# Kernel optimization log

Measured on AMD Instinct MI355X. Metric: run time of the kernel, lower is better.

Reference implementation:

```python
import jax, jax.numpy as jnp
import numpy as np

HUGE = 1e9  # stand-in for ops.HUGE_INT


def setup_inputs() -> dict:
    key = jax.random.key(0)
    ks = jax.random.split(key, 8)
    B, Q, K = 8, 128, 256
    Dq = Dk = Dv = H = 512
    query = jax.random.normal(ks[0], (B, Q, Dq), dtype=jnp.float32)
    k_ = jax.random.normal(ks[1], (B, K, Dk), dtype=jnp.float32)
    value = jax.random.normal(ks[2], (B, K, Dv), dtype=jnp.float32)
    mask = jax.random.randint(ks[3], (B, K), 0, 2, dtype=jnp.int32)
    # FFN params: linear1 (Dq+Dk -> H, bias), linear2 (H -> 1, no bias)
    W1 = jax.random.normal(ks[4], (Dq + Dk, H), dtype=jnp.float32) * 0.05
    b1 = jax.random.normal(ks[5], (H,), dtype=jnp.float32) * 0.05
    w2 = jax.random.normal(ks[6], (H, 1), dtype=jnp.float32) * 0.05
    return {"query": query, "key": k_, "value": value, "mask": mask,
            "W1": W1, "b1": b1, "w2": w2}


def reference(query, key, value, mask, W1, b1, w2):
    # Additive (FFN) attention. Original tiles query/key into [B, Q*K, Dq+Dk]
    # and applies linear1; concat@W1 is separable, so we project q and k
    # separately and broadcast-add (same math, no tiled concat tensor).
    Dq = query.shape[-1]
    Wq, Wk = W1[:Dq], W1[Dq:]
    q_proj = jnp.einsum('bqd,dh->bqh', query, Wq)   # [B,Q,H]
    k_proj = jnp.einsum('bkd,dh->bkh', key, Wk)     # [B,K,H]
    hidden = jnp.tanh(q_proj[:, :, None, :] + k_proj[:, None, :, :] + b1)  # [B,Q,K,H]
    scores = jnp.einsum('bqkh,h->bqk', hidden, w2[:, 0])  # [B,Q,K]
    # padding mask fill BEFORE scaling, matching the original op order
    scores = jnp.where(mask[:, None, :] != 0, -HUGE, scores)
    scores = scores / jnp.sqrt(jnp.float32(key.shape[-1]))
    attn_weights = jax.nn.softmax(scores, axis=-1)
    attn_vec = jnp.einsum('bqk,bkv->bqv', attn_weights, value)  # dropout=0 at eval
    return attn_vec, attn_weights
```

## Files before the change

kernel.cpp:

```cpp
#include <hip/hip_runtime.h>
#include <hip/hip_bf16.h>

#define B_ 8
#define Q_ 128
#define K_ 256
#define D_ 512
#define TWOLOG2E 2.8853900817779268f
#define SCALE 0.044194173824159216f
#define L2E 1.4426950408889634f
#define MASKVAL (-44194173.824159216f)

typedef __attribute__((ext_vector_type(8))) short frag8;
typedef __attribute__((ext_vector_type(4))) float f32x4;

__device__ __forceinline__ float fexp2(float x) {
  float r;
  asm("v_exp_f32 %0, %1" : "=v"(r) : "v"(x));
  return r;
}
__device__ __forceinline__ float frcp(float x) {
  float r;
  asm("v_rcp_f32 %0, %1" : "=v"(r) : "v"(x));
  return r;
}
__device__ __forceinline__ unsigned f2bf_u(float x) {
  unsigned u = __float_as_uint(x);
  return (u + 0x7FFFu + ((u >> 16) & 1u)) >> 16;
}
__device__ __forceinline__ unsigned short f2bf(float x) {
  return (unsigned short)f2bf_u(x);
}
__device__ __forceinline__ unsigned packbf(float lo, float hi) {
  return f2bf_u(lo) | (f2bf_u(hi) << 16);
}

__global__ __launch_bounds__(256) void gemm_kernel(
    const float* __restrict__ query, const float* __restrict__ key,
    const float* __restrict__ W1, const float* __restrict__ b1,
    float* __restrict__ qp, float* __restrict__ kpbT) {
  __shared__ short As[32 * 64];
  __shared__ short Bs[64 * 72];
  const int t = threadIdx.x;
  const int m0 = blockIdx.y * 32;
  const int n0 = blockIdx.x * 64;
  const bool is_k = (m0 >= B_ * Q_);
  const float* X = is_k ? key : query;
  const int xrow0 = is_k ? (m0 - B_ * Q_) : m0;
  const float* Wb = W1 + (is_k ? (size_t)D_ * D_ : 0);

  const int am = t >> 3;
  const int ac = t & 7;
  const float* gA = X + (size_t)(xrow0 + am) * D_ + ac * 8;
  short* aw = As + am * 64 + ((ac ^ (am & 7)) * 8);

  const int prow = t >> 4;
  const int n4 = (t & 15) * 4;
  const float* gB = Wb + n0 + n4;

  const int l = t & 63;
  const int w = t >> 6;
  const int lr = l & 15;
  const int kg = l >> 4;
  const int key8 = lr & 7;
  int aoff[2][2], boff[2];
#pragma unroll
  for (int kk = 0; kk < 2; ++kk) {
    const int cposA = ((kg + kk * 4) ^ key8) * 8;
#pragma unroll
    for (int mt = 0; mt < 2; ++mt) aoff[mt][kk] = (mt * 16 + lr) * 64 + cposA;
    boff[kk] = (w * 16 + lr) * 72 + (kg + kk * 4) * 8;
  }

  f32x4 acc[2];
  acc[0] = (f32x4){0.f, 0.f, 0.f, 0.f};
  acc[1] = (f32x4){0.f, 0.f, 0.f, 0.f};

  for (int k0 = 0; k0 < D_; k0 += 64) {
    float4 a0 = *(const float4*)(gA + k0);
    float4 a1 = *(const float4*)(gA + k0 + 4);
    float4 w00 = *(const float4*)(gB + (size_t)(k0 + 2 * prow) * D_);
    float4 w01 = *(const float4*)(gB + (size_t)(k0 + 2 * prow + 1) * D_);
    float4 w10 = *(const float4*)(gB + (size_t)(k0 + 2 * prow + 32) * D_);
    float4 w11 = *(const float4*)(gB + (size_t)(k0 + 2 * prow + 33) * D_);
    __syncthreads();
    {
      union { frag8 f; unsigned short u[8]; } av;
      av.u[0] = f2bf(a0.x); av.u[1] = f2bf(a0.y); av.u[2] = f2bf(a0.z); av.u[3] = f2bf(a0.w);
      av.u[4] = f2bf(a1.x); av.u[5] = f2bf(a1.y); av.u[6] = f2bf(a1.z); av.u[7] = f2bf(a1.w);
      *(frag8*)aw = av.f;
    }
    {
      float lo0[4] = {w00.x, w00.y, w00.z, w00.w};
      float hi0[4] = {w01.x, w01.y, w01.z, w01.w};
      float lo1[4] = {w10.x, w10.y, w10.z, w10.w};
      float hi1[4] = {w11.x, w11.y, w11.z, w11.w};
#pragma unroll
      for (int j = 0; j < 4; ++j) {
        *(unsigned*)(Bs + (n4 + j) * 72 + 2 * prow) = packbf(lo0[j], hi0[j]);
        *(unsigned*)(Bs + (n4 + j) * 72 + 2 * (prow + 16)) = packbf(lo1[j], hi1[j]);
      }
    }
    __syncthreads();
#pragma unroll
    for (int kk = 0; kk < 2; ++kk) {
      frag8 bf = *(const frag8*)(Bs + boff[kk]);
#pragma unroll
      for (int mt = 0; mt < 2; ++mt) {
        frag8 af = *(const frag8*)(As + aoff[mt][kk]);
        acc[mt] = __builtin_amdgcn_mfma_f32_16x16x32_bf16(af, bf, acc[mt], 0, 0, 0);
      }
    }
  }

  const int col = n0 + w * 16 + lr;
  if (is_k) {
    const float bc = b1[col];
#pragma unroll
    for (int mt = 0; mt < 2; ++mt) {
      const int krow = m0 - B_ * Q_ + mt * 16 + kg * 4;
      const int bb = krow >> 8;
      const int kk0 = krow & 255;
      float4 v;
      v.x = fexp2((acc[mt][0] + bc) * TWOLOG2E);
      v.y = fexp2((acc[mt][1] + bc) * TWOLOG2E);
      v.z = fexp2((acc[mt][2] + bc) * TWOLOG2E);
      v.w = fexp2((acc[mt][3] + bc) * TWOLOG2E);
      *(float4*)&kpbT[((size_t)bb * D_ + col) * K_ + kk0] = v;
    }
  } else {
#pragma unroll
    for (int mt = 0; mt < 2; ++mt) {
#pragma unroll
      for (int i = 0; i < 4; ++i) {
        const int row = m0 + mt * 16 + kg * 4 + i;
        qp[(size_t)row * D_ + col] = fexp2(acc[mt][i] * TWOLOG2E);
      }
    }
  }
}

__global__ __launch_bounds__(1024) void attn_kernel(
    const float* __restrict__ qp, const float* __restrict__ kpbT,
    const float* __restrict__ value, const int* __restrict__ mask,
    const float* __restrict__ w2,
    float* __restrict__ out_vec, float* __restrict__ out_w) {
  __shared__ float smem_p[16 * 512];
  __shared__ float pw[4 * 256];
  const int bid = blockIdx.x;
  const int b = bid & 7;
  const int q0 = (bid >> 3) * 4;
  const int t = threadIdx.x;
  const int lane = t & 63;
  const int w = __builtin_amdgcn_readfirstlane(t >> 6);
  const int kc = w & 1;
  const int hq = w >> 1;
  const int h0 = hq * 64;

  {
    const float* pk = kpbT + ((size_t)b * D_ + h0) * K_ + kc * 128 + 2 * lane;
    const float* q_0 = qp + (size_t)(b * Q_ + q0 + 0) * D_ + h0;
    const float* q_1 = qp + (size_t)(b * Q_ + q0 + 1) * D_ + h0;
    const float* q_2 = qp + (size_t)(b * Q_ + q0 + 2) * D_ + h0;
    const float* q_3 = qp + (size_t)(b * Q_ + q0 + 3) * D_ + h0;
    const float* w2h = w2 + h0;

    float2 a0 = {0.f, 0.f}, a1 = {0.f, 0.f}, a2 = {0.f, 0.f}, a3 = {0.f, 0.f};
    for (int h = 0; h < 64; h += 8) {
      float2 kv[8];
#pragma unroll
      for (int j = 0; j < 8; ++j) kv[j] = *(const float2*)&pk[(size_t)(h + j) * K_];
      float4 e0a = *(const float4*)(q_0 + h), e0b = *(const float4*)(q_0 + h + 4);
      float4 e1a = *(const float4*)(q_1 + h), e1b = *(const float4*)(q_1 + h + 4);
      float4 e2a = *(const float4*)(q_2 + h), e2b = *(const float4*)(q_2 + h + 4);
      float4 e3a = *(const float4*)(q_3 + h), e3b = *(const float4*)(q_3 + h + 4);
      float4 wa = *(const float4*)(w2h + h), wb = *(const float4*)(w2h + h + 4);
      float E0[8] = {e0a.x, e0a.y, e0a.z, e0a.w, e0b.x, e0b.y, e0b.z, e0b.w};
      float E1[8] = {e1a.x, e1a.y, e1a.z, e1a.w, e1b.x, e1b.y, e1b.z, e1b.w};
      float E2[8] = {e2a.x, e2a.y, e2a.z, e2a.w, e2b.x, e2b.y, e2b.z, e2b.w};
      float E3[8] = {e3a.x, e3a.y, e3a.z, e3a.w, e3b.x, e3b.y, e3b.z, e3b.w};
      float WV[8] = {wa.x, wa.y, wa.z, wa.w, wb.x, wb.y, wb.z, wb.w};
#pragma unroll
      for (int p = 0; p < 4; ++p) {
        const int j0 = 2 * p, j1 = 2 * p + 1;
        const float w0 = WV[j0], w1 = WV[j1];
        {
          float d0x = fmaf(E0[j0], kv[j0].x, 1.f), d1x = fmaf(E0[j1], kv[j1].x, 1.f);
          float d0y = fmaf(E0[j0], kv[j0].y, 1.f), d1y = fmaf(E0[j1], kv[j1].y, 1.f);
          a0.x = fmaf(fmaf(w0, d1x, w1 * d0x), frcp(d0x * d1x), a0.x);
          a0.y = fmaf(fmaf(w0, d1y, w1 * d0y), frcp(d0y * d1y), a0.y);
        }
        {
          float d0x = fmaf(E1[j0], kv[j0].x, 1.f), d1x = fmaf(E1[j1], kv[j1].x, 1.f);
          float d0y = fmaf(E1[j0], kv[j0].y, 1.f), d1y = fmaf(E1[j1], kv[j1].y, 1.f);
          a1.x = fmaf(fmaf(w0, d1x, w1 * d0x), frcp(d0x * d1x), a1.x);
          a1.y = fmaf(fmaf(w0, d1y, w1 * d0y), frcp(d0y * d1y), a1.y);
        }
        {
          float d0x = fmaf(E2[j0], kv[j0].x, 1.f), d1x = fmaf(E2[j1], kv[j1].x, 1.f);
          float d0y = fmaf(E2[j0], kv[j0].y, 1.f), d1y = fmaf(E2[j1], kv[j1].y, 1.f);
          a2.x = fmaf(fmaf(w0, d1x, w1 * d0x), frcp(d0x * d1x), a2.x);
          a2.y = fmaf(fmaf(w0, d1y, w1 * d0y), frcp(d0y * d1y), a2.y);
        }
        {
          float d0x = fmaf(E3[j0], kv[j0].x, 1.f), d1x = fmaf(E3[j1], kv[j1].x, 1.f);
          float d0y = fmaf(E3[j0], kv[j0].y, 1.f), d1y = fmaf(E3[j1], kv[j1].y, 1.f);
          a3.x = fmaf(fmaf(w0, d1x, w1 * d0x), frcp(d0x * d1x), a3.x);
          a3.y = fmaf(fmaf(w0, d1y, w1 * d0y), frcp(d0y * d1y), a3.y);
        }
      }
    }
    *(float2*)&smem_p[w * 512 + 0 * 128 + 2 * lane] = a0;
    *(float2*)&smem_p[w * 512 + 1 * 128 + 2 * lane] = a1;
    *(float2*)&smem_p[w * 512 + 2 * 128 + 2 * lane] = a2;
    *(float2*)&smem_p[w * 512 + 3 * 128 + 2 * lane] = a3;
  }
  __syncthreads();

  if (w < 4) {
    const int q = w;
    float sw = 0.f;
#pragma unroll
    for (int m = 0; m < 8; ++m) sw += w2[lane + 64 * m];
#pragma unroll
    for (int off = 32; off; off >>= 1) sw += __shfl_xor(sw, off);

    float s[4];
#pragma unroll
    for (int r = 0; r < 4; ++r) {
      const int kcc = r >> 1;
      const int off = (r & 1) * 64 + lane;
      float p = 0.f;
#pragma unroll
      for (int hh = 0; hh < 8; ++hh)
        p += smem_p[(hh * 2 + kcc) * 512 + q * 128 + off];
      const int mk = mask[b * K_ + r * 64 + lane];
      s[r] = mk ? MASKVAL : fmaf(-2.f, p, sw) * SCALE;
    }
    float mx = fmaxf(fmaxf(s[0], s[1]), fmaxf(s[2], s[3]));
#pragma unroll
    for (int off = 32; off; off >>= 1) mx = fmaxf(mx, __shfl_xor(mx, off));
    float e[4], sum = 0.f;
#pragma unroll
    for (int r = 0; r < 4; ++r) {
      e[r] = fexp2((s[r] - mx) * L2E);
      sum += e[r];
    }
#pragma unroll
    for (int off = 32; off; off >>= 1) sum += __shfl_xor(sum, off);
    const float inv = frcp(sum);
    float* ow = out_w + (size_t)(b * Q_ + q0 + q) * K_;
#pragma unroll
    for (int r = 0; r < 4; ++r) {
      const float p = e[r] * inv;
      pw[q * 256 + r * 64 + lane] = p;
      ow[r * 64 + lane] = p;
    }
  }
  __syncthreads();

  {
    const int cp = t & 255;
    const int col = cp * 2;
    const int kq = t >> 8;
    const float* vb = value + (size_t)b * K_ * D_ + (size_t)(kq * 64) * D_ + col;
    const float* pwq = pw + kq * 64;

    float2 o0 = {0.f, 0.f}, o1 = {0.f, 0.f}, o2 = {0.f, 0.f}, o3 = {0.f, 0.f};
    for (int k0 = 0; k0 < 64; k0 += 4) {
      const float4 P0 = *(const float4*)&pwq[0 * 256 + k0];
      const float4 P1 = *(const float4*)&pwq[1 * 256 + k0];
      const float4 P2 = *(const float4*)&pwq[2 * 256 + k0];
      const float4 P3 = *(const float4*)&pwq[3 * 256 + k0];
      const float2 v0 = *(const float2*)&vb[(size_t)(k0 + 0) * D_];
      const float2 v1 = *(const float2*)&vb[(size_t)(k0 + 1) * D_];
      const float2 v2 = *(const float2*)&vb[(size_t)(k0 + 2) * D_];
      const float2 v3 = *(const float2*)&vb[(size_t)(k0 + 3) * D_];
      o0.x = fmaf(P0.x, v0.x, fmaf(P0.y, v1.x, fmaf(P0.z, v2.x, fmaf(P0.w, v3.x, o0.x))));
      o0.y = fmaf(P0.x, v0.y, fmaf(P0.y, v1.y, fmaf(P0.z, v2.y, fmaf(P0.w, v3.y, o0.y))));
      o1.x = fmaf(P1.x, v0.x, fmaf(P1.y, v1.x, fmaf(P1.z, v2.x, fmaf(P1.w, v3.x, o1.x))));
      o1.y = fmaf(P1.x, v0.y, fmaf(P1.y, v1.y, fmaf(P1.z, v2.y, fmaf(P1.w, v3.y, o1.y))));
      o2.x = fmaf(P2.x, v0.x, fmaf(P2.y, v1.x, fmaf(P2.z, v2.x, fmaf(P2.w, v3.x, o2.x))));
      o2.y = fmaf(P2.x, v0.y, fmaf(P2.y, v1.y, fmaf(P2.z, v2.y, fmaf(P2.w, v3.y, o2.y))));
      o3.x = fmaf(P3.x, v0.x, fmaf(P3.y, v1.x, fmaf(P3.z, v2.x, fmaf(P3.w, v3.x, o3.x))));
      o3.y = fmaf(P3.x, v0.y, fmaf(P3.y, v1.y, fmaf(P3.z, v2.y, fmaf(P3.w, v3.y, o3.y))));
    }
    __syncthreads();
    *(float2*)&smem_p[kq * 2048 + 0 * 512 + col] = o0;
    *(float2*)&smem_p[kq * 2048 + 1 * 512 + col] = o1;
    *(float2*)&smem_p[kq * 2048 + 2 * 512 + col] = o2;
    *(float2*)&smem_p[kq * 2048 + 3 * 512 + col] = o3;
  }
  __syncthreads();

  {
#pragma unroll
    for (int rep = 0; rep < 2; ++rep) {
      const int idx = t + rep * 1024;
      const int q = idx >> 9;
      const int c = idx & 511;
      const float s = smem_p[0 * 2048 + q * 512 + c] + smem_p[1 * 2048 + q * 512 + c] +
                      smem_p[2 * 2048 + q * 512 + c] + smem_p[3 * 2048 + q * 512 + c];
      out_vec[(size_t)(b * Q_ + q0 + q) * D_ + c] = s;
    }
  }
}

extern "C" void kernel_launch(void* const* d_in, const int* in_sizes, int n_in,
                              void* d_out, int out_size, void* d_ws, size_t ws_size,
                              hipStream_t stream) {
  const float* query = (const float*)d_in[0];
  const float* key   = (const float*)d_in[1];
  const float* value = (const float*)d_in[2];
  const int*   mask  = (const int*)d_in[3];
  const float* W1    = (const float*)d_in[4];
  const float* b1    = (const float*)d_in[5];
  const float* w2    = (const float*)d_in[6];

  float* out_vec = (float*)d_out;
  float* out_w   = out_vec + (size_t)B_ * Q_ * D_;

  float* qp   = (float*)d_ws;
  float* kpbT = qp + (size_t)B_ * Q_ * D_;

  gemm_kernel<<<dim3(8, 96), 256, 0, stream>>>(query, key, W1, b1, qp, kpbT);
  attn_kernel<<<dim3(256), 1024, 0, stream>>>(qp, kpbT, value, mask, w2,
                                              out_vec, out_w);
}
```

Before: 106.2 us.

## Compact unmasked keys and skip score computation for masked keys

One wave compacts the indices of unmasked keys into shared memory with a ballot and prefix-popcount. The score loop now runs only over the compacted keys, gathering key projections by index. The hidden dimension is re-split across all 16 waves, 32 each, instead of a 2x8 key/hidden split. Softmax runs over the compacted positions and the probabilities are scattered back to their original key slots, with zeros elsewhere. This trades about half the tanh-style work on random masks for uncoalesced gathered loads and an extra scatter pass; if every key is masked, the result becomes all-zero weights instead of uniform ones.

```diff
diff --git a/kernel.cpp b/kernel.cpp
--- a/kernel.cpp
+++ b/kernel.cpp
@@ -144,75 +144,95 @@
     const float* __restrict__ value, const int* __restrict__ mask,
     const float* __restrict__ w2,
     float* __restrict__ out_vec, float* __restrict__ out_w) {
-  __shared__ float smem_p[16 * 512];
+  __shared__ float smem_p[16 * 4 * 256];
   __shared__ float pw[4 * 256];
+  __shared__ int ck[K_];
+  __shared__ int nk_sh;
   const int bid = blockIdx.x;
   const int b = bid & 7;
   const int q0 = (bid >> 3) * 4;
   const int t = threadIdx.x;
   const int lane = t & 63;
   const int w = __builtin_amdgcn_readfirstlane(t >> 6);
-  const int kc = w & 1;
-  const int hq = w >> 1;
-  const int h0 = hq * 64;
+
+  if (t < 64) {
+    int base = 0;
+#pragma unroll
+    for (int r = 0; r < 4; ++r) {
+      const int k = r * 64 + lane;
+      const bool um = (mask[b * K_ + k] == 0);
+      const unsigned long long bal = __ballot(um);
+      if (um) ck[base + __popcll(bal & ((1ull << lane) - 1ull))] = k;
+      base += (int)__popcll(bal);
+    }
+    if (lane == 0) nk_sh = base;
+  }
+  __syncthreads();
+  const int nk = nk_sh;
+  const int npass = (nk + 63) >> 6;
 
   {
-    const float* pk = kpbT + ((size_t)b * D_ + h0) * K_ + kc * 128 + 2 * lane;
-    const float* q_0 = qp + (size_t)(b * Q_ + q0 + 0) * D_ + h0;
-    const float* q_1 = qp + (size_t)(b * Q_ + q0 + 1) * D_ + h0;
-    const float* q_2 = qp + (size_t)(b * Q_ + q0 + 2) * D_ + h0;
-    const float* q_3 = qp + (size_t)(b * Q_ + q0 + 3) * D_ + h0;
-    const float* w2h = w2 + h0;
-
-    float2 a0 = {0.f, 0.f}, a1 = {0.f, 0.f}, a2 = {0.f, 0.f}, a3 = {0.f, 0.f};
-    for (int h = 0; h < 64; h += 8) {
-      float2 kv[8];
-#pragma unroll
-      for (int j = 0; j < 8; ++j) kv[j] = *(const float2*)&pk[(size_t)(h + j) * K_];
-      float4 e0a = *(const float4*)(q_0 + h), e0b = *(const float4*)(q_0 + h + 4);
-      float4 e1a = *(const float4*)(q_1 + h), e1b = *(const float4*)(q_1 + h + 4);
-      float4 e2a = *(const float4*)(q_2 + h), e2b = *(const float4*)(q_2 + h + 4);
-      float4 e3a = *(const float4*)(q_3 + h), e3b = *(const float4*)(q_3 + h + 4);
-      float4 wa = *(const float4*)(w2h + h), wb = *(const float4*)(w2h + h + 4);
-      float E0[8] = {e0a.x, e0a.y, e0a.z, e0a.w, e0b.x, e0b.y, e0b.z, e0b.w};
-      float E1[8] = {e1a.x, e1a.y, e1a.z, e1a.w, e1b.x, e1b.y, e1b.z, e1b.w};
-      float E2[8] = {e2a.x, e2a.y, e2a.z, e2a.w, e2b.x, e2b.y, e2b.z, e2b.w};
-      float E3[8] = {e3a.x, e3a.y, e3a.z, e3a.w, e3b.x, e3b.y, e3b.z, e3b.w};
-      float WV[8] = {wa.x, wa.y, wa.z, wa.w, wb.x, wb.y, wb.z, wb.w};
+    const int h0p = w * 32;
+    const float* pkrow = kpbT + ((size_t)b * D_ + h0p) * K_;
+    const float* q_0 = qp + (size_t)(b * Q_ + q0 + 0) * D_ + h0p;
+    const float* q_1 = qp + (size_t)(b * Q_ + q0 + 1) * D_ + h0p;
+    const float* q_2 = qp + (size_t)(b * Q_ + q0 + 2) * D_ + h0p;
+    const float* q_3 = qp + (size_t)(b * Q_ + q0 + 3) * D_ + h0p;
+    const float* w2h = w2 + h0p;
+
+    int kidx[4];
+#pragma unroll
+    for (int p = 0; p < 4; ++p) {
+      const int pos = p * 64 + lane;
+      kidx[p] = (pos < nk) ? ck[pos] : 0;
+    }
+
+    float acc[4][4];
+#pragma unroll
+    for (int p = 0; p < 4; ++p)
+#pragma unroll
+      for (int qi = 0; qi < 4; ++qi) acc[p][qi] = 0.f;
+
+    for (int h = 0; h < 32; h += 2) {
+      const float2 wv = *(const float2*)(w2h + h);
+      const float2 e0 = *(const float2*)(q_0 + h);
+      const float2 e1 = *(const float2*)(q_1 + h);
+      const float2 e2 = *(const float2*)(q_2 + h);
+      const float2 e3 = *(const float2*)(q_3 + h);
+      const float* ra = pkrow + (size_t)h * K_;
+      const float* rb = ra + K_;
 #pragma unroll
       for (int p = 0; p < 4; ++p) {
-        const int j0 = 2 * p, j1 = 2 * p + 1;
-        const float w0 = WV[j0], w1 = WV[j1];
-        {
-          float d0x = fmaf(E0[j0], kv[j0].x, 1.f), d1x = fmaf(E0[j1], kv[j1].x, 1.f);
-          float d0y = fmaf(E0[j0], kv[j0].y, 1.f), d1y = fmaf(E0[j1], kv[j1].y, 1.f);
-          a0.x = fmaf(fmaf(w0, d1x, w1 * d0x), frcp(d0x * d1x), a0.x);
-          a0.y = fmaf(fmaf(w0, d1y, w1 * d0y), frcp(d0y * d1y), a0.y);
+        if (p < npass) {
+          const float eka = ra[kidx[p]];
+          const float ekb = rb[kidx[p]];
+          {
+            const float da = fmaf(e0.x, eka, 1.f), db = fmaf(e0.y, ekb, 1.f);
+            acc[p][0] = fmaf(fmaf(wv.x, db, wv.y * da), frcp(da * db), acc[p][0]);
+          }
+          {
+            const float da = fmaf(e1.x, eka, 1.f), db = fmaf(e1.y, ekb, 1.f);
+            acc[p][1] = fmaf(fmaf(wv.x, db, wv.y * da), frcp(da * db), acc[p][1]);
+          }
+          {
+            const float da = fmaf(e2.x, eka, 1.f), db = fmaf(e2.y, ekb, 1.f);
+            acc[p][2] = fmaf(fmaf(wv.x, db, wv.y * da), frcp(da * db), acc[p][2]);
+          }
+          {
+            const float da = fmaf(e3.x, eka, 1.f), db = fmaf(e3.y, ekb, 1.f);
+            acc[p][3] = fmaf(fmaf(wv.x, db, wv.y * da), frcp(da * db), acc[p][3]);
+          }
         }
-        {
-          float d0x = fmaf(E1[j0], kv[j0].x, 1.f), d1x = fmaf(E1[j1], kv[j1].x, 1.f);
-          float d0y = fmaf(E1[j0], kv[j0].y, 1.f), d1y = fmaf(E1[j1], kv[j1].y, 1.f);
-          a1.x = fmaf(fmaf(w0, d1x, w1 * d0x), frcp(d0x * d1x), a1.x);
-          a1.y = fmaf(fmaf(w0, d1y, w1 * d0y), frcp(d0y * d1y), a1.y);
-        }
-        {
-          float d0x = fmaf(E2[j0], kv[j0].x, 1.f), d1x = fmaf(E2[j1], kv[j1].x, 1.f);
-          float d0y = fmaf(E2[j0], kv[j0].y, 1.f), d1y = fmaf(E2[j1], kv[j1].y, 1.f);
-          a2.x = fmaf(fmaf(w0, d1x, w1 * d0x), frcp(d0x * d1x), a2.x);
-          a2.y = fmaf(fmaf(w0, d1y, w1 * d0y), frcp(d0y * d1y), a2.y);
-        }
-        {
-          float d0x = fmaf(E3[j0], kv[j0].x, 1.f), d1x = fmaf(E3[j1], kv[j1].x, 1.f);
-          float d0y = fmaf(E3[j0], kv[j0].y, 1.f), d1y = fmaf(E3[j1], kv[j1].y, 1.f);
-          a3.x = fmaf(fmaf(w0, d1x, w1 * d0x), frcp(d0x * d1x), a3.x);
-          a3.y = fmaf(fmaf(w0, d1y, w1 * d0y), frcp(d0y * d1y), a3.y);
-        }
-      }
-    }
-    *(float2*)&smem_p[w * 512 + 0 * 128 + 2 * lane] = a0;
-    *(float2*)&smem_p[w * 512 + 1 * 128 + 2 * lane] = a1;
-    *(float2*)&smem_p[w * 512 + 2 * 128 + 2 * lane] = a2;
-    *(float2*)&smem_p[w * 512 + 3 * 128 + 2 * lane] = a3;
+      }
+    }
+#pragma unroll
+    for (int p = 0; p < 4; ++p) {
+      if (p < npass) {
+#pragma unroll
+        for (int qi = 0; qi < 4; ++qi)
+          smem_p[(w * 4 + qi) * 256 + p * 64 + lane] = acc[p][qi];
+      }
+    }
   }
   __syncthreads();
 
@@ -227,14 +247,11 @@
     float s[4];
 #pragma unroll
     for (int r = 0; r < 4; ++r) {
-      const int kcc = r >> 1;
-      const int off = (r & 1) * 64 + lane;
+      const int pos = r * 64 + lane;
       float p = 0.f;
 #pragma unroll
-      for (int hh = 0; hh < 8; ++hh)
-        p += smem_p[(hh * 2 + kcc) * 512 + q * 128 + off];
-      const int mk = mask[b * K_ + r * 64 + lane];
-      s[r] = mk ? MASKVAL : fmaf(-2.f, p, sw) * SCALE;
+      for (int wv = 0; wv < 16; ++wv) p += smem_p[(wv * 4 + q) * 256 + pos];
+      s[r] = (pos < nk) ? fmaf(-2.f, p, sw) * SCALE : MASKVAL;
     }
     float mx = fmaxf(fmaxf(s[0], s[1]), fmaxf(s[2], s[3]));
 #pragma unroll
@@ -248,13 +265,16 @@
 #pragma unroll
     for (int off = 32; off; off >>= 1) sum += __shfl_xor(sum, off);
     const float inv = frcp(sum);
+#pragma unroll
+    for (int r = 0; r < 4; ++r) pw[q * 256 + r * 64 + lane] = 0.f;
+#pragma unroll
+    for (int r = 0; r < 4; ++r) {
+      const int pos = r * 64 + lane;
+      if (pos < nk) pw[q * 256 + ck[pos]] = e[r] * inv;
+    }
     float* ow = out_w + (size_t)(b * Q_ + q0 + q) * K_;
 #pragma unroll
-    for (int r = 0; r < 4; ++r) {
-      const float p = e[r] * inv;
-      pw[q * 256 + r * 64 + lane] = p;
-      ow[r * 64 + lane] = p;
-    }
+    for (int r = 0; r < 4; ++r) ow[r * 64 + lane] = pw[q * 256 + r * 64 + lane];
   }
   __syncthreads();
 
```

Result: slower. 112.3 us (+5.7%).
